# Kernel tuning notes

Hardware: AMD Instinct MI355X
Metric: run time of the kernel (lower is better)

## Reference

```python
import jax, jax.numpy as jnp
import numpy as np

N = 50000
E = 800000
D = 128
L = 2


def setup_inputs() -> dict:
    key = jax.random.key(0)
    ks = jax.random.split(key, 8)
    x = jax.random.normal(ks[0], (N, D), dtype=jnp.float32)
    edge_index = jax.random.randint(ks[1], (2, E), 0, N, dtype=jnp.int64)
    s = 1.0 / np.sqrt(D)
    Wl = jax.random.uniform(ks[2], (L, D, D), jnp.float32, -s, s)  # neighbor transform (with bias)
    bl = jax.random.uniform(ks[3], (L, D), jnp.float32, -s, s)
    Wr = jax.random.uniform(ks[4], (L, D, D), jnp.float32, -s, s)  # root/self transform (no bias)
    W = jax.random.uniform(ks[5], (D, D), jnp.float32, -s, s)      # final Linear
    b = jax.random.uniform(ks[6], (D,), jnp.float32, -s, s)
    return {"x": x, "edge_index": edge_index, "Wl": Wl, "bl": bl, "Wr": Wr, "W": W, "b": b}


def reference(x, edge_index, Wl, bl, Wr, W, b):
    src, dst = edge_index[0], edge_index[1]
    n = x.shape[0]
    for l in range(Wl.shape[0]):
        # gather neighbor (source) features, scatter-max into destination nodes
        agg = jax.ops.segment_max(x[src], dst, num_segments=n)  # [N, D]
        agg = jnp.where(jnp.isneginf(agg), 0.0, agg)  # PyG: isolated nodes -> 0
        # SAGEConv: lin_l(agg) + lin_r(x)
        x = agg @ Wl[l].T + bl[l] + x @ Wr[l].T
        x = jax.nn.relu(x)
    return x @ W.T + b
```

## Files before the change

kernel.cpp:

```cpp
#include <hip/hip_runtime.h>
#include <math.h>

#define NN 50000
#define NE 800000
#define DD 128
#define NBUCK 196
#define EPB 2048
#define PB 391
#define CONVB 6250

typedef unsigned short u16;
typedef short s8v __attribute__((ext_vector_type(8)));
typedef float f16v __attribute__((ext_vector_type(16)));

__device__ __forceinline__ u16 f2bf(float f) {
    unsigned u = __float_as_uint(f);
    return (u16)((u + 0x7FFFu + ((u >> 16) & 1u)) >> 16);
}
__device__ __forceinline__ float bflo(unsigned u) { return __uint_as_float(u << 16); }
__device__ __forceinline__ float bfhi(unsigned u) { return __uint_as_float(u & 0xFFFF0000u); }

__global__ __launch_bounds__(256) void zero_kernel(int* __restrict__ p, int n) {
    int i = threadIdx.x + blockIdx.x * 256;
    if (i < n) p[i] = 0;
}

__device__ __forceinline__ void pack_one(const float* __restrict__ Wl,
                                         const float* __restrict__ Wr,
                                         bool two, int o, u16* __restrict__ out) {
    int j = o & 7;
    int l = (o >> 3) & 63;
    int cn = o >> 9;
    int n = cn & 3;
    int c = cn >> 2;
    int colj = n * 32 + (l & 31);
    int k = c * 16 + (l >> 5) * 8 + j;
    float v;
    if (two) v = (k < DD) ? Wl[colj * DD + k] : Wr[colj * DD + (k - DD)];
    else     v = Wl[colj * DD + k];
    out[o] = f2bf(v);
}

__global__ __launch_bounds__(256) void prep_kernel(
        const float4* __restrict__ x4, ushort4* __restrict__ hb0,
        const float* __restrict__ Wl, const float* __restrict__ Wr,
        const float* __restrict__ W,
        u16* __restrict__ Bpk0, u16* __restrict__ Bpk1, u16* __restrict__ Bpkf,
        const int* __restrict__ ei, int* __restrict__ bcnt) {
    int bid = blockIdx.x;
    int tid = threadIdx.x;
    if (bid < CONVB) {
        int i = bid * 256 + tid;
        float4 v = x4[i];
        ushort4 o;
        o.x = f2bf(v.x); o.y = f2bf(v.y); o.z = f2bf(v.z); o.w = f2bf(v.w);
        hb0[i] = o;
    } else if (bid < CONVB + 128) {
        pack_one(Wl, Wr, true, (bid - CONVB) * 256 + tid, Bpk0);
    } else if (bid < CONVB + 256) {
        pack_one(Wl + DD * DD, Wr + DD * DD, true, (bid - CONVB - 128) * 256 + tid, Bpk1);
    } else if (bid < CONVB + 320) {
        pack_one(W, W, false, (bid - CONVB - 256) * 256 + tid, Bpkf);
    } else {
        __shared__ int h[NBUCK];
        for (int i = tid; i < NBUCK; i += 256) h[i] = 0;
        __syncthreads();
        int e0 = (bid - (CONVB + 320)) * EPB;
#pragma unroll
        for (int i = 0; i < 8; i++) {
            int e = e0 + i * 256 + tid;
            if (e < NE) atomicAdd(&h[ei[NE + e] >> 8], 1);
        }
        __syncthreads();
        for (int i = tid; i < NBUCK; i += 256)
            if (h[i]) atomicAdd(&bcnt[i], h[i]);
    }
}

__global__ __launch_bounds__(256) void bucket_partition(const int* __restrict__ ei,
                                                        const int* __restrict__ bcnt,
                                                        int* __restrict__ claim,
                                                        unsigned* __restrict__ packed,
                                                        int* __restrict__ rowptr) {
    __shared__ int sc[256];
    __shared__ int bb[NBUCK];
    __shared__ int h[NBUCK];
    __shared__ int base[NBUCK];
    int t = threadIdx.x;
    int v = (t < NBUCK) ? bcnt[t] : 0;
    sc[t] = v;
    __syncthreads();
    for (int o = 1; o < 256; o <<= 1) {
        int u = (t >= o) ? sc[t - o] : 0;
        __syncthreads();
        sc[t] += u;
        __syncthreads();
    }
    if (t < NBUCK) bb[t] = sc[t] - v;
    if (t == 0 && blockIdx.x == 0) rowptr[NN] = NE;
    for (int i = t; i < NBUCK; i += 256) h[i] = 0;
    __syncthreads();
    int e0 = blockIdx.x * EPB;
    int dsts[8], srcs[8];
#pragma unroll
    for (int i = 0; i < 8; i++) {
        int e = e0 + i * 256 + t;
        if (e < NE) {
            dsts[i] = ei[NE + e];
            srcs[i] = ei[e];
            atomicAdd(&h[dsts[i] >> 8], 1);
        } else dsts[i] = -1;
    }
    __syncthreads();
    for (int i = t; i < NBUCK; i += 256) {
        int c = h[i];
        base[i] = c ? bb[i] + atomicAdd(&claim[i], c) : 0;
    }
    __syncthreads();
    for (int i = t; i < NBUCK; i += 256) h[i] = 0;
    __syncthreads();
#pragma unroll
    for (int i = 0; i < 8; i++) {
        if (dsts[i] >= 0) {
            int bk = dsts[i] >> 8;
            int r = atomicAdd(&h[bk], 1);
            packed[base[bk] + r] = (unsigned)srcs[i] | ((unsigned)(dsts[i] & 255) << 16);
        }
    }
}

__global__ __launch_bounds__(256) void bucket_csr(const unsigned* __restrict__ packed,
                                                  const int* __restrict__ bcnt,
                                                  int* __restrict__ rowptr,
                                                  int* __restrict__ col) {
    __shared__ int sc[256];
    __shared__ int deg[256];
    __shared__ int off[256];
    int t = threadIdx.x;
    int v0 = (t < NBUCK) ? bcnt[t] : 0;
    sc[t] = v0;
    __syncthreads();
    for (int o = 1; o < 256; o <<= 1) {
        int u = (t >= o) ? sc[t - o] : 0;
        __syncthreads();
        sc[t] += u;
        __syncthreads();
    }
    int bk = blockIdx.x;
    int cnt = bcnt[bk];
    int base = sc[bk] - cnt;
    deg[t] = 0;
    __syncthreads();
    for (int i = t; i < cnt; i += 256) atomicAdd(&deg[packed[base + i] >> 16], 1);
    __syncthreads();
    int v = deg[t];
    off[t] = v;
    __syncthreads();
    for (int o = 1; o < 256; o <<= 1) {
        int u = (t >= o) ? off[t - o] : 0;
        __syncthreads();
        off[t] += u;
        __syncthreads();
    }
    int ex = off[t] - v;
    int node = (bk << 8) + t;
    if (node < NN) rowptr[node] = base + ex;
    deg[t] = ex;
    __syncthreads();
    for (int i = t; i < cnt; i += 256) {
        unsigned p = packed[base + i];
        int dl = p >> 16;
        int r = atomicAdd(&deg[dl], 1);
        col[base + r] = (int)(p & 0xFFFFu);
    }
}

__device__ __forceinline__ void vmax8(float* m, uint4 v) {
    m[0] = fmaxf(m[0], bflo(v.x)); m[1] = fmaxf(m[1], bfhi(v.x));
    m[2] = fmaxf(m[2], bflo(v.y)); m[3] = fmaxf(m[3], bfhi(v.y));
    m[4] = fmaxf(m[4], bflo(v.z)); m[5] = fmaxf(m[5], bfhi(v.z));
    m[6] = fmaxf(m[6], bflo(v.w)); m[7] = fmaxf(m[7], bfhi(v.w));
}

__global__ __launch_bounds__(256) void agg_kernel_bf(const uint4* __restrict__ xb4,
                                                     const int* __restrict__ row_ptr,
                                                     const int* __restrict__ col,
                                                     uint4* __restrict__ aggb4) {
    int node = blockIdx.x * 16 + (threadIdx.x >> 4);
    if (node >= NN) return;
    int j = threadIdx.x & 15;
    int s0 = row_ptr[node], s1 = row_ptr[node + 1];
    if (s0 == s1) {
        aggb4[(size_t)node * 16 + j] = make_uint4(0, 0, 0, 0);
        return;
    }
    float m0[8], m1[8], m2[8], m3[8];
#pragma unroll
    for (int q = 0; q < 8; q++) { m0[q] = m1[q] = m2[q] = m3[q] = -INFINITY; }
    int i = s0;
    for (; i + 8 <= s1; i += 8) {
        int c0 = col[i],     c1 = col[i + 1], c2 = col[i + 2], c3 = col[i + 3];
        int c4 = col[i + 4], c5 = col[i + 5], c6 = col[i + 6], c7 = col[i + 7];
        uint4 v0 = xb4[(size_t)c0 * 16 + j];
        uint4 v1 = xb4[(size_t)c1 * 16 + j];
        uint4 v2 = xb4[(size_t)c2 * 16 + j];
        uint4 v3 = xb4[(size_t)c3 * 16 + j];
        uint4 v4 = xb4[(size_t)c4 * 16 + j];
        uint4 v5 = xb4[(size_t)c5 * 16 + j];
        uint4 v6 = xb4[(size_t)c6 * 16 + j];
        uint4 v7 = xb4[(size_t)c7 * 16 + j];
        vmax8(m0, v0); vmax8(m1, v1); vmax8(m2, v2); vmax8(m3, v3);
        vmax8(m0, v4); vmax8(m1, v5); vmax8(m2, v6); vmax8(m3, v7);
    }
    for (; i + 4 <= s1; i += 4) {
        int c0 = col[i], c1 = col[i + 1], c2 = col[i + 2], c3 = col[i + 3];
        uint4 v0 = xb4[(size_t)c0 * 16 + j];
        uint4 v1 = xb4[(size_t)c1 * 16 + j];
        uint4 v2 = xb4[(size_t)c2 * 16 + j];
        uint4 v3 = xb4[(size_t)c3 * 16 + j];
        vmax8(m0, v0); vmax8(m1, v1); vmax8(m2, v2); vmax8(m3, v3);
    }
    for (; i < s1; i++) {
        uint4 v = xb4[(size_t)col[i] * 16 + j];
        vmax8(m0, v);
    }
#pragma unroll
    for (int q = 0; q < 8; q++) m0[q] = fmaxf(fmaxf(m0[q], m1[q]), fmaxf(m2[q], m3[q]));
    uint4 o;
    o.x = (__float_as_uint(m0[0]) >> 16) | (__float_as_uint(m0[1]) & 0xFFFF0000u);
    o.y = (__float_as_uint(m0[2]) >> 16) | (__float_as_uint(m0[3]) & 0xFFFF0000u);
    o.z = (__float_as_uint(m0[4]) >> 16) | (__float_as_uint(m0[5]) & 0xFFFF0000u);
    o.w = (__float_as_uint(m0[6]) >> 16) | (__float_as_uint(m0[7]) & 0xFFFF0000u);
    aggb4[(size_t)node * 16 + j] = o;
}

__global__ __launch_bounds__(256) void mfma_gemm0(const u16* __restrict__ srcA,
                                                  const u16* __restrict__ srcB,
                                                  const u16* __restrict__ Bpk,
                                                  const float* __restrict__ bias,
                                                  u16* __restrict__ outh) {
    int tid = threadIdx.x;
    int wt = tid >> 6;
    int lane = tid & 63;
    int row0 = blockIdx.x * 128 + wt * 32;
    int rload = row0 + (lane & 31);
    if (rload > NN - 1) rload = NN - 1;
    int koff = (lane >> 5) * 8;
    const s8v* Bv = (const s8v*)Bpk;

    f16v acc[4];
#pragma unroll
    for (int n = 0; n < 4; n++) acc[n] = (f16v)(0.0f);

#pragma unroll
    for (int c = 0; c < 16; c++) {
        const u16* s = srcA;
        int kk = c * 16;
        if (c >= 8) { s = srcB; kk = (c - 8) * 16; }
        s8v a = *(const s8v*)(s + (size_t)rload * DD + kk + koff);
#pragma unroll
        for (int n = 0; n < 4; n++) {
            s8v b = Bv[(c * 4 + n) * 64 + lane];
            acc[n] = __builtin_amdgcn_mfma_f32_32x32x16_bf16(a, b, acc[n], 0, 0, 0);
        }
    }

    int rowadd = 4 * (lane >> 5);
#pragma unroll
    for (int n = 0; n < 4; n++) {
        int colj = n * 32 + (lane & 31);
        float bj = bias[colj];
#pragma unroll
        for (int r = 0; r < 16; r++) {
            int row = row0 + (r & 3) + 8 * (r >> 2) + rowadd;
            if (row < NN)
                outh[(size_t)row * DD + colj] = f2bf(fmaxf(acc[n][r] + bj, 0.0f));
        }
    }
}

__global__ __launch_bounds__(256) void gemm_final(const u16* __restrict__ srcA,
                                                  const u16* __restrict__ srcB,
                                                  const u16* __restrict__ Bpk,
                                                  const float* __restrict__ bias,
                                                  const u16* __restrict__ Bpkf,
                                                  const float* __restrict__ bfin,
                                                  float* __restrict__ out) {
    __shared__ u16 As[128 * 128];
    char* Ab = (char*)As;
    int tid = threadIdx.x;
    int wt = tid >> 6;
    int lane = tid & 63;
    int row0 = blockIdx.x * 128;
    int arl = wt * 32 + (lane & 31);
    int rg = row0 + arl;
    if (rg > NN - 1) rg = NN - 1;
    int koff = (lane >> 5) * 8;
    int swz = (arl & 7) << 4;
    const s8v* Bv = (const s8v*)Bpk;

    f16v acc[4];
#pragma unroll
    for (int n = 0; n < 4; n++) acc[n] = (f16v)(0.0f);

#pragma unroll
    for (int c = 0; c < 16; c++) {
        const u16* s = srcA;
        int kk = c * 16;
        if (c >= 8) { s = srcB; kk = (c - 8) * 16; }
        s8v a = *(const s8v*)(s + (size_t)rg * DD + kk + koff);
#pragma unroll
        for (int n = 0; n < 4; n++) {
            s8v b = Bv[(c * 4 + n) * 64 + lane];
            acc[n] = __builtin_amdgcn_mfma_f32_32x32x16_bf16(a, b, acc[n], 0, 0, 0);
        }
    }

    int rowadd = 4 * (lane >> 5);
#pragma unroll
    for (int n = 0; n < 4; n++) {
        int colj = n * 32 + (lane & 31);
        float bj = bias[colj];
#pragma unroll
        for (int r = 0; r < 16; r++) {
            int rloc = wt * 32 + (r & 3) + 8 * (r >> 2) + rowadd;
            float v = fmaxf(acc[n][r] + bj, 0.0f);
            *(u16*)(Ab + rloc * 256 + ((colj * 2) ^ ((rloc & 7) << 4))) = f2bf(v);
        }
    }
    __syncthreads();

    const s8v* Bvf = (const s8v*)Bpkf;
    f16v acc2[4];
#pragma unroll
    for (int n = 0; n < 4; n++) acc2[n] = (f16v)(0.0f);
#pragma unroll
    for (int c = 0; c < 8; c++) {
        s8v a = *(const s8v*)(Ab + arl * 256 + (((c * 16 + koff) * 2) ^ swz));
#pragma unroll
        for (int n = 0; n < 4; n++) {
            s8v b = Bvf[(c * 4 + n) * 64 + lane];
            acc2[n] = __builtin_amdgcn_mfma_f32_32x32x16_bf16(a, b, acc2[n], 0, 0, 0);
        }
    }
#pragma unroll
    for (int n = 0; n < 4; n++) {
        int colj = n * 32 + (lane & 31);
        float bj = bfin[colj];
#pragma unroll
        for (int r = 0; r < 16; r++) {
            int row = row0 + wt * 32 + (r & 3) + 8 * (r >> 2) + rowadd;
            if (row < NN)
                out[(size_t)row * DD + colj] = acc2[n][r] + bj;
        }
    }
}

extern "C" void kernel_launch(void* const* d_in, const int* in_sizes, int n_in,
                              void* d_out, int out_size, void* d_ws, size_t ws_size,
                              hipStream_t stream) {
    const float* x  = (const float*)d_in[0];
    const int*   ei = (const int*)d_in[1];
    const float* Wl = (const float*)d_in[2];
    const float* bl = (const float*)d_in[3];
    const float* Wr = (const float*)d_in[4];
    const float* W  = (const float*)d_in[5];
    const float* b  = (const float*)d_in[6];
    float* out = (float*)d_out;

    u16* aggb = (u16*)d_ws;
    u16* hb0  = aggb + (size_t)NN * DD;
    u16* hb1  = hb0 + (size_t)NN * DD;
    u16* Bpk0 = hb1 + (size_t)NN * DD;
    u16* Bpk1 = Bpk0 + 32768;
    u16* Bpkf = Bpk1 + 32768;
    unsigned* packed = (unsigned*)(Bpkf + 16384);
    int* col    = (int*)(packed + NE);
    int* rowptr = col + NE;
    int* bcnt   = rowptr + NN + 1;
    int* claim  = bcnt + NBUCK;

    dim3 blk(256);
    int gemmBlocks = (NN + 127) / 128;
    int aggBlocks  = (NN + 15) / 16;
    int prepBlocks = CONVB + 320 + PB;

    zero_kernel<<<2, blk, 0, stream>>>(bcnt, 2 * NBUCK);
    prep_kernel<<<prepBlocks, blk, 0, stream>>>(
        (const float4*)x, (ushort4*)hb0, Wl, Wr, W, Bpk0, Bpk1, Bpkf, ei, bcnt);

    bucket_partition<<<PB, blk, 0, stream>>>(ei, bcnt, claim, packed, rowptr);
    bucket_csr<<<NBUCK, blk, 0, stream>>>(packed, bcnt, rowptr, col);

    agg_kernel_bf<<<aggBlocks, blk, 0, stream>>>((const uint4*)hb0, rowptr, col, (uint4*)aggb);
    mfma_gemm0<<<gemmBlocks, blk, 0, stream>>>(aggb, hb0, Bpk0, bl, hb1);

    agg_kernel_bf<<<aggBlocks, blk, 0, stream>>>((const uint4*)hb1, rowptr, col, (uint4*)aggb);
    gemm_final<<<gemmBlocks, blk, 0, stream>>>(aggb, hb1, Bpk1, bl + DD, Bpkf, b, out);
}
```

Baseline: 235.8 us.

## Aggregate over feature-chunked transposed layout to shrink gather working set

Adds a second copy of the node features stored as four 32-feature chunks, each a contiguous [N,32] slab, written by the prep kernel and by the first GEMM epilogue. The GEMM now stages its output tile in swizzled shared memory and writes both layouts with 8-byte stores. The new aggregation kernel gives each block one feature chunk over 64 nodes, so concurrently running blocks gather from a 3.2 MB slab rather than the full feature matrix, which is meant to improve cache hit rates for the random neighbour gathers. The cost is extra writes of the transposed copy, more workspace memory, and reading the CSR column indices four times instead of once.

After: 238.5 us. About the same (+1.2%).

```diff
diff --git a/kernel.cpp b/kernel.cpp
--- a/kernel.cpp
+++ b/kernel.cpp
@@ -8,8 +8,10 @@
 #define EPB 2048
 #define PB 391
 #define CONVB 6250
+#define NTILE 782
 
 typedef unsigned short u16;
+typedef unsigned long long u64t;
 typedef short s8v __attribute__((ext_vector_type(8)));
 typedef float f16v __attribute__((ext_vector_type(16)));
 
@@ -43,6 +45,7 @@
 
 __global__ __launch_bounds__(256) void prep_kernel(
         const float4* __restrict__ x4, ushort4* __restrict__ hb0,
+        ushort4* __restrict__ hbT,
         const float* __restrict__ Wl, const float* __restrict__ Wr,
         const float* __restrict__ W,
         u16* __restrict__ Bpk0, u16* __restrict__ Bpk1, u16* __restrict__ Bpkf,
@@ -55,6 +58,8 @@
         ushort4 o;
         o.x = f2bf(v.x); o.y = f2bf(v.y); o.z = f2bf(v.z); o.w = f2bf(v.w);
         hb0[i] = o;
+        int node = i >> 5, pos = i & 31;
+        hbT[((size_t)((pos >> 3) * NN + node) << 3) + (pos & 7)] = o;
     } else if (bid < CONVB + 128) {
         pack_one(Wl, Wr, true, (bid - CONVB) * 256 + tid, Bpk0);
     } else if (bid < CONVB + 256) {
@@ -182,68 +187,72 @@
     m[6] = fmaxf(m[6], bflo(v.w)); m[7] = fmaxf(m[7], bfhi(v.w));
 }
 
-__global__ __launch_bounds__(256) void agg_kernel_bf(const uint4* __restrict__ xb4,
-                                                     const int* __restrict__ row_ptr,
-                                                     const int* __restrict__ col,
-                                                     uint4* __restrict__ aggb4) {
-    int node = blockIdx.x * 16 + (threadIdx.x >> 4);
+__global__ __launch_bounds__(256) void agg_chunked(const uint4* __restrict__ hbT4,
+                                                   const int* __restrict__ rowptr,
+                                                   const int* __restrict__ col,
+                                                   uint4* __restrict__ aggb4) {
+    int bid = blockIdx.x;
+    int chunk = (bid & 7) >> 1;
+    int ntile = ((bid >> 3) << 1) | (bid & 1);
+    int t = threadIdx.x;
+    int node = ntile * 64 + (t >> 2);
+    int q = t & 3;
     if (node >= NN) return;
-    int j = threadIdx.x & 15;
-    int s0 = row_ptr[node], s1 = row_ptr[node + 1];
-    if (s0 == s1) {
-        aggb4[(size_t)node * 16 + j] = make_uint4(0, 0, 0, 0);
-        return;
-    }
-    float m0[8], m1[8], m2[8], m3[8];
-#pragma unroll
-    for (int q = 0; q < 8; q++) { m0[q] = m1[q] = m2[q] = m3[q] = -INFINITY; }
-    int i = s0;
-    for (; i + 8 <= s1; i += 8) {
-        int c0 = col[i],     c1 = col[i + 1], c2 = col[i + 2], c3 = col[i + 3];
-        int c4 = col[i + 4], c5 = col[i + 5], c6 = col[i + 6], c7 = col[i + 7];
-        uint4 v0 = xb4[(size_t)c0 * 16 + j];
-        uint4 v1 = xb4[(size_t)c1 * 16 + j];
-        uint4 v2 = xb4[(size_t)c2 * 16 + j];
-        uint4 v3 = xb4[(size_t)c3 * 16 + j];
-        uint4 v4 = xb4[(size_t)c4 * 16 + j];
-        uint4 v5 = xb4[(size_t)c5 * 16 + j];
-        uint4 v6 = xb4[(size_t)c6 * 16 + j];
-        uint4 v7 = xb4[(size_t)c7 * 16 + j];
-        vmax8(m0, v0); vmax8(m1, v1); vmax8(m2, v2); vmax8(m3, v3);
-        vmax8(m0, v4); vmax8(m1, v5); vmax8(m2, v6); vmax8(m3, v7);
-    }
-    for (; i + 4 <= s1; i += 4) {
-        int c0 = col[i], c1 = col[i + 1], c2 = col[i + 2], c3 = col[i + 3];
-        uint4 v0 = xb4[(size_t)c0 * 16 + j];
-        uint4 v1 = xb4[(size_t)c1 * 16 + j];
-        uint4 v2 = xb4[(size_t)c2 * 16 + j];
-        uint4 v3 = xb4[(size_t)c3 * 16 + j];
-        vmax8(m0, v0); vmax8(m1, v1); vmax8(m2, v2); vmax8(m3, v3);
-    }
-    for (; i < s1; i++) {
-        uint4 v = xb4[(size_t)col[i] * 16 + j];
-        vmax8(m0, v);
-    }
-#pragma unroll
-    for (int q = 0; q < 8; q++) m0[q] = fmaxf(fmaxf(m0[q], m1[q]), fmaxf(m2[q], m3[q]));
-    uint4 o;
-    o.x = (__float_as_uint(m0[0]) >> 16) | (__float_as_uint(m0[1]) & 0xFFFF0000u);
-    o.y = (__float_as_uint(m0[2]) >> 16) | (__float_as_uint(m0[3]) & 0xFFFF0000u);
-    o.z = (__float_as_uint(m0[4]) >> 16) | (__float_as_uint(m0[5]) & 0xFFFF0000u);
-    o.w = (__float_as_uint(m0[6]) >> 16) | (__float_as_uint(m0[7]) & 0xFFFF0000u);
-    aggb4[(size_t)node * 16 + j] = o;
+    const uint4* src4 = hbT4 + ((size_t)chunk * NN) * 4 + q;
+    int s0 = rowptr[node], s1 = rowptr[node + 1];
+    uint4 o = make_uint4(0u, 0u, 0u, 0u);
+    if (s0 < s1) {
+        float m0[8], m1[8];
+#pragma unroll
+        for (int k = 0; k < 8; k++) { m0[k] = m1[k] = -INFINITY; }
+        int i = s0;
+        for (; i + 8 <= s1; i += 8) {
+            int c0 = col[i],     c1 = col[i + 1], c2 = col[i + 2], c3 = col[i + 3];
+            int c4 = col[i + 4], c5 = col[i + 5], c6 = col[i + 6], c7 = col[i + 7];
+            uint4 v0 = src4[(size_t)c0 * 4];
+            uint4 v1 = src4[(size_t)c1 * 4];
+            uint4 v2 = src4[(size_t)c2 * 4];
+            uint4 v3 = src4[(size_t)c3 * 4];
+            uint4 v4 = src4[(size_t)c4 * 4];
+            uint4 v5 = src4[(size_t)c5 * 4];
+            uint4 v6 = src4[(size_t)c6 * 4];
+            uint4 v7 = src4[(size_t)c7 * 4];
+            vmax8(m0, v0); vmax8(m1, v1); vmax8(m0, v2); vmax8(m1, v3);
+            vmax8(m0, v4); vmax8(m1, v5); vmax8(m0, v6); vmax8(m1, v7);
+        }
+        for (; i + 2 <= s1; i += 2) {
+            int c0 = col[i], c1 = col[i + 1];
+            uint4 v0 = src4[(size_t)c0 * 4];
+            uint4 v1 = src4[(size_t)c1 * 4];
+            vmax8(m0, v0); vmax8(m1, v1);
+        }
+        if (i < s1) {
+            uint4 v = src4[(size_t)col[i] * 4];
+            vmax8(m0, v);
+        }
+#pragma unroll
+        for (int k = 0; k < 8; k++) m0[k] = fmaxf(m0[k], m1[k]);
+        o.x = (__float_as_uint(m0[0]) >> 16) | (__float_as_uint(m0[1]) & 0xFFFF0000u);
+        o.y = (__float_as_uint(m0[2]) >> 16) | (__float_as_uint(m0[3]) & 0xFFFF0000u);
+        o.z = (__float_as_uint(m0[4]) >> 16) | (__float_as_uint(m0[5]) & 0xFFFF0000u);
+        o.w = (__float_as_uint(m0[6]) >> 16) | (__float_as_uint(m0[7]) & 0xFFFF0000u);
+    }
+    aggb4[(size_t)node * 16 + chunk * 4 + q] = o;
 }
 
 __global__ __launch_bounds__(256) void mfma_gemm0(const u16* __restrict__ srcA,
                                                   const u16* __restrict__ srcB,
                                                   const u16* __restrict__ Bpk,
                                                   const float* __restrict__ bias,
-                                                  u16* __restrict__ outh) {
+                                                  u16* __restrict__ outh,
+                                                  u16* __restrict__ outT) {
+    __shared__ u16 As[128 * 128];
+    char* Ab = (char*)As;
     int tid = threadIdx.x;
     int wt = tid >> 6;
     int lane = tid & 63;
-    int row0 = blockIdx.x * 128 + wt * 32;
-    int rload = row0 + (lane & 31);
+    int row0 = blockIdx.x * 128;
+    int rload = row0 + wt * 32 + (lane & 31);
     if (rload > NN - 1) rload = NN - 1;
     int koff = (lane >> 5) * 8;
     const s8v* Bv = (const s8v*)Bpk;
@@ -272,9 +281,23 @@
         float bj = bias[colj];
 #pragma unroll
         for (int r = 0; r < 16; r++) {
-            int row = row0 + (r & 3) + 8 * (r >> 2) + rowadd;
-            if (row < NN)
-                outh[(size_t)row * DD + colj] = f2bf(fmaxf(acc[n][r] + bj, 0.0f));
+            int rloc = wt * 32 + (r & 3) + 8 * (r >> 2) + rowadd;
+            float v = fmaxf(acc[n][r] + bj, 0.0f);
+            *(u16*)(Ab + rloc * 256 + ((colj * 2) ^ ((rloc & 7) << 4))) = f2bf(v);
+        }
+    }
+    __syncthreads();
+
+#pragma unroll
+    for (int it = 0; it < 16; it++) {
+        int flat = it * 256 + tid;
+        int rl = flat >> 5;
+        int p  = flat & 31;
+        u64t v = *(const u64t*)(Ab + rl * 256 + ((p * 8) ^ ((rl & 7) << 4)));
+        int row = row0 + rl;
+        if (row < NN) {
+            *(u64t*)(outh + (size_t)row * DD + p * 4) = v;
+            *(u64t*)(outT + (((size_t)((p >> 3) * NN + row)) << 5) + (p & 7) * 4) = v;
         }
     }
 }
@@ -371,7 +394,8 @@
     u16* aggb = (u16*)d_ws;
     u16* hb0  = aggb + (size_t)NN * DD;
     u16* hb1  = hb0 + (size_t)NN * DD;
-    u16* Bpk0 = hb1 + (size_t)NN * DD;
+    u16* hbT  = hb1 + (size_t)NN * DD;
+    u16* Bpk0 = hbT + (size_t)NN * DD;
     u16* Bpk1 = Bpk0 + 32768;
     u16* Bpkf = Bpk1 + 32768;
     unsigned* packed = (unsigned*)(Bpkf + 16384);
@@ -382,19 +406,20 @@
 
     dim3 blk(256);
     int gemmBlocks = (NN + 127) / 128;
-    int aggBlocks  = (NN + 15) / 16;
+    int aggBlocks  = NTILE * 4;
     int prepBlocks = CONVB + 320 + PB;
 
     zero_kernel<<<2, blk, 0, stream>>>(bcnt, 2 * NBUCK);
     prep_kernel<<<prepBlocks, blk, 0, stream>>>(
-        (const float4*)x, (ushort4*)hb0, Wl, Wr, W, Bpk0, Bpk1, Bpkf, ei, bcnt);
+        (const float4*)x, (ushort4*)hb0, (ushort4*)hbT, Wl, Wr, W,
+        Bpk0, Bpk1, Bpkf, ei, bcnt);
 
     bucket_partition<<<PB, blk, 0, stream>>>(ei, bcnt, claim, packed, rowptr);
     bucket_csr<<<NBUCK, blk, 0, stream>>>(packed, bcnt, rowptr, col);
 
-    agg_kernel_bf<<<aggBlocks, blk, 0, stream>>>((const uint4*)hb0, rowptr, col, (uint4*)aggb);
-    mfma_gemm0<<<gemmBlocks, blk, 0, stream>>>(aggb, hb0, Bpk0, bl, hb1);
-
-    agg_kernel_bf<<<aggBlocks, blk, 0, stream>>>((const uint4*)hb1, rowptr, col, (uint4*)aggb);
+    agg_chunked<<<aggBlocks, blk, 0, stream>>>((const uint4*)hbT, rowptr, col, (uint4*)aggb);
+    mfma_gemm0<<<gemmBlocks, blk, 0, stream>>>(aggb, hb0, Bpk0, bl, hb1, hbT);
+
+    agg_chunked<<<aggBlocks, blk, 0, stream>>>((const uint4*)hbT, rowptr, col, (uint4*)aggb);
     gemm_final<<<gemmBlocks, blk, 0, stream>>>(aggb, hb1, Bpk1, bl + DD, Bpkf, b, out);
 }
```

## Stage GEMM epilogue through swizzled LDS for coalesced stores; deepen gather unroll

Applied to the files above, without the earlier changes.

The first-layer MFMA GEMM epilogue now writes its bf16 results into a 32KB XOR-swizzled shared-memory tile, then copies the tile out as coalesced 8-byte stores. This replaces the scattered 2-byte-per-lane global writes. The max-aggregation gather also gains a 16-way unrolled loop so more neighbor loads are in flight per thread. The costs are extra LDS use, which may lower occupancy, a block-wide barrier, and higher register pressure from the 16 uint4 buffers.

Result: no change. 237.9 us (+0.9%).

```diff
diff --git a/kernel.cpp b/kernel.cpp
--- a/kernel.cpp
+++ b/kernel.cpp
@@ -10,6 +10,7 @@
 #define CONVB 6250
 
 typedef unsigned short u16;
+typedef unsigned long long u64t;
 typedef short s8v __attribute__((ext_vector_type(8)));
 typedef float f16v __attribute__((ext_vector_type(16)));
 
@@ -198,26 +199,35 @@
 #pragma unroll
     for (int q = 0; q < 8; q++) { m0[q] = m1[q] = m2[q] = m3[q] = -INFINITY; }
     int i = s0;
+    for (; i + 16 <= s1; i += 16) {
+        uint4 vv[16];
+#pragma unroll
+        for (int k = 0; k < 16; k++) vv[k] = xb4[(size_t)col[i + k] * 16 + j];
+#pragma unroll
+        for (int k = 0; k < 16; k++) {
+            if ((k & 3) == 0) vmax8(m0, vv[k]);
+            else if ((k & 3) == 1) vmax8(m1, vv[k]);
+            else if ((k & 3) == 2) vmax8(m2, vv[k]);
+            else vmax8(m3, vv[k]);
+        }
+    }
     for (; i + 8 <= s1; i += 8) {
-        int c0 = col[i],     c1 = col[i + 1], c2 = col[i + 2], c3 = col[i + 3];
-        int c4 = col[i + 4], c5 = col[i + 5], c6 = col[i + 6], c7 = col[i + 7];
-        uint4 v0 = xb4[(size_t)c0 * 16 + j];
-        uint4 v1 = xb4[(size_t)c1 * 16 + j];
-        uint4 v2 = xb4[(size_t)c2 * 16 + j];
-        uint4 v3 = xb4[(size_t)c3 * 16 + j];
-        uint4 v4 = xb4[(size_t)c4 * 16 + j];
-        uint4 v5 = xb4[(size_t)c5 * 16 + j];
-        uint4 v6 = xb4[(size_t)c6 * 16 + j];
-        uint4 v7 = xb4[(size_t)c7 * 16 + j];
-        vmax8(m0, v0); vmax8(m1, v1); vmax8(m2, v2); vmax8(m3, v3);
-        vmax8(m0, v4); vmax8(m1, v5); vmax8(m2, v6); vmax8(m3, v7);
+        uint4 vv[8];
+#pragma unroll
+        for (int k = 0; k < 8; k++) vv[k] = xb4[(size_t)col[i + k] * 16 + j];
+#pragma unroll
+        for (int k = 0; k < 8; k++) {
+            if ((k & 3) == 0) vmax8(m0, vv[k]);
+            else if ((k & 3) == 1) vmax8(m1, vv[k]);
+            else if ((k & 3) == 2) vmax8(m2, vv[k]);
+            else vmax8(m3, vv[k]);
+        }
     }
     for (; i + 4 <= s1; i += 4) {
-        int c0 = col[i], c1 = col[i + 1], c2 = col[i + 2], c3 = col[i + 3];
-        uint4 v0 = xb4[(size_t)c0 * 16 + j];
-        uint4 v1 = xb4[(size_t)c1 * 16 + j];
-        uint4 v2 = xb4[(size_t)c2 * 16 + j];
-        uint4 v3 = xb4[(size_t)c3 * 16 + j];
+        uint4 v0 = xb4[(size_t)col[i] * 16 + j];
+        uint4 v1 = xb4[(size_t)col[i + 1] * 16 + j];
+        uint4 v2 = xb4[(size_t)col[i + 2] * 16 + j];
+        uint4 v3 = xb4[(size_t)col[i + 3] * 16 + j];
         vmax8(m0, v0); vmax8(m1, v1); vmax8(m2, v2); vmax8(m3, v3);
     }
     for (; i < s1; i++) {
@@ -239,11 +249,13 @@
                                                   const u16* __restrict__ Bpk,
                                                   const float* __restrict__ bias,
                                                   u16* __restrict__ outh) {
+    __shared__ u16 As[128 * 128];
+    char* Ab = (char*)As;
     int tid = threadIdx.x;
     int wt = tid >> 6;
     int lane = tid & 63;
-    int row0 = blockIdx.x * 128 + wt * 32;
-    int rload = row0 + (lane & 31);
+    int row0 = blockIdx.x * 128;
+    int rload = row0 + wt * 32 + (lane & 31);
     if (rload > NN - 1) rload = NN - 1;
     int koff = (lane >> 5) * 8;
     const s8v* Bv = (const s8v*)Bpk;
@@ -272,10 +284,22 @@
         float bj = bias[colj];
 #pragma unroll
         for (int r = 0; r < 16; r++) {
-            int row = row0 + (r & 3) + 8 * (r >> 2) + rowadd;
-            if (row < NN)
-                outh[(size_t)row * DD + colj] = f2bf(fmaxf(acc[n][r] + bj, 0.0f));
-        }
+            int rloc = wt * 32 + (r & 3) + 8 * (r >> 2) + rowadd;
+            float v = fmaxf(acc[n][r] + bj, 0.0f);
+            *(u16*)(Ab + rloc * 256 + ((colj * 2) ^ ((rloc & 7) << 4))) = f2bf(v);
+        }
+    }
+    __syncthreads();
+
+#pragma unroll
+    for (int it = 0; it < 16; it++) {
+        int flat = it * 256 + tid;
+        int rl = flat >> 5;
+        int p  = flat & 31;
+        u64t v = *(const u64t*)(Ab + rl * 256 + ((p * 8) ^ ((rl & 7) << 4)));
+        int row = row0 + rl;
+        if (row < NN)
+            *(u64t*)(outh + (size_t)row * DD + p * 4) = v;
     }
 }
 
```
